# Performance work log

Hardware: AMD Instinct MI355X
Metric: run time of the kernel (lower is better)

## Reference

```python
import jax, jax.numpy as jnp
import numpy as np
from jax import lax

N_QUBITS = 4
DIM = 2 ** N_QUBITS  # 16-amplitude state vector


def _cnot_perm(c, t):
    # CNOT(control=c, target=t): amp_out[j] = amp_in[j ^ (bit_c(j) * mask_t)]
    idx = np.arange(DIM)
    mc = 1 << (N_QUBITS - 1 - c)  # PennyLane: wire 0 is most significant
    mt = 1 << (N_QUBITS - 1 - t)
    return jnp.asarray(np.where(idx & mc, idx ^ mt, idx))

# BasicEntanglerLayers ring pattern for n>2: CNOT(0,1),(1,2),(2,3),(3,0)
CNOT_PERMS = [_cnot_perm(i, (i + 1) % N_QUBITS) for i in range(N_QUBITS)]
_bits = (np.arange(DIM)[None, :] >> (N_QUBITS - 1 - np.arange(N_QUBITS)[:, None])) & 1
Z_SIGNS = jnp.asarray(1.0 - 2.0 * _bits, dtype=jnp.float32)  # [4,16], PauliZ eigenvalues


def _apply_1q(state, U, wire):
    # state: [B, 16] complex; U: [2,2] (shared) or [B,2,2] (per-sample angle)
    B = state.shape[0]
    s = state.reshape(B, 2 ** wire, 2, 2 ** (N_QUBITS - 1 - wire))
    if U.ndim == 2:
        s = jnp.einsum('ij,bajc->baic', U, s)
    else:
        s = jnp.einsum('bij,bajc->baic', U, s)
    return s.reshape(B, DIM)


def quantum_circuit(inputs, weights):
    # Batched default.qubit simulation. inputs: [B,4] angles, weights: [3,4].
    B = inputs.shape[0]
    state = jnp.zeros((B, DIM), jnp.complex64).at[:, 0].set(1.0)
    # RY(inputs[:,w]) on each wire (per-sample angles)
    for w in range(N_QUBITS):
        th = inputs[:, w] * 0.5
        c = jnp.cos(th).astype(jnp.complex64)
        s = jnp.sin(th).astype(jnp.complex64)
        U = jnp.stack([jnp.stack([c, -s], -1), jnp.stack([s, c], -1)], -2)  # [B,2,2]
        state = _apply_1q(state, U, w)
    # BasicEntanglerLayers: per layer, RX(weights[l,w]) on each wire then CNOT ring
    for l in range(weights.shape[0]):
        for w in range(N_QUBITS):
            th = weights[l, w] * 0.5
            cc = jnp.cos(th).astype(jnp.complex64)
            ss = (-1j) * jnp.sin(th).astype(jnp.complex64)
            U = jnp.stack([jnp.stack([cc, ss]), jnp.stack([ss, cc])])  # [2,2]
            state = _apply_1q(state, U, w)
        for w in range(N_QUBITS):
            state = state[:, CNOT_PERMS[w]]
    probs = jnp.abs(state) ** 2  # [B,16]
    return (probs @ Z_SIGNS.T).astype(jnp.float32)  # [B,4] <Z_w>


def setup_inputs() -> dict:
    key = jax.random.key(0)
    ks = jax.random.split(key, 8)
    B = 16384
    return {
        'x': jax.random.normal(ks[0], (B, 3, 32, 32), jnp.float32),
        'conv_w': jax.random.normal(ks[1], (N_QUBITS, 3, 3, 3), jnp.float32) * 0.1,
        'conv_b': jnp.zeros((N_QUBITS,), jnp.float32),
        'q_weights': jax.random.normal(ks[2], (3, N_QUBITS), jnp.float32),
        'w1': jax.random.normal(ks[3], (128, N_QUBITS), jnp.float32) * 0.1,
        'b1': jnp.zeros((128,), jnp.float32),
        'w2': jax.random.normal(ks[4], (3 * 32 * 32, 128), jnp.float32) * 0.05,
        'b2': jnp.zeros((3 * 32 * 32,), jnp.float32),
    }


def reference(x, conv_w, conv_b, q_weights, w1, b1, w2, b2):
    # Conv2d(3, 4, k=3, pad=1)
    y = lax.conv_general_dilated(
        x, conv_w, window_strides=(1, 1), padding='SAME',
        dimension_numbers=('NCHW', 'OIHW', 'NCHW')) + conv_b[None, :, None, None]
    # adaptive_avg_pool2d to (1,1) == global mean over H,W -> [B,4]
    pooled = y.mean(axis=(2, 3))
    # per-sample quantum circuit, batched; torch.tensor() in the original
    # detaches gradients, mirrored by stop_gradient
    q = lax.stop_gradient(quantum_circuit(pooled, q_weights))
    h = jax.nn.relu(q @ w1.T + b1)
    out = h @ w2.T + b2
    return out.reshape(-1, 3, 32, 32)
```

## Files before the change

### kernel.cpp

```cpp
#include <hip/hip_runtime.h>
#include <hip/hip_bf16.h>

typedef __attribute__((ext_vector_type(8))) short bf16x8;
typedef __attribute__((ext_vector_type(4))) float f32x4;

__device__ __forceinline__ unsigned short f2bf(float f) {
  union { __hip_bfloat16 b; unsigned short u; } cv;
  cv.b = __float2bfloat16(f);
  return cv.u;
}

__global__ __launch_bounds__(256) void k_cvt_w2(const float* __restrict__ w2,
                                                unsigned short* __restrict__ w2b) {
  const int i = (blockIdx.x * 256 + threadIdx.x) * 4;
  float4 v = *(const float4*)(w2 + i);
  union { uint2 u; unsigned short s[4]; } p;
  p.s[0] = f2bf(v.x); p.s[1] = f2bf(v.y); p.s[2] = f2bf(v.z); p.s[3] = f2bf(v.w);
  *(uint2*)(w2b + i) = p.u;
}

__global__ __launch_bounds__(64) void k_convpool(const float* __restrict__ x,
                                                 const float* __restrict__ cw,
                                                 const float* __restrict__ cb,
                                                 float* __restrict__ pooled) {
  const int b = blockIdx.x;
  const int t = threadIdx.x;
  const float4* x4 = (const float4*)x + (size_t)b * 768;
  float F[3] = {0,0,0}, R0[3] = {0,0,0}, R31[3] = {0,0,0}, C0[3] = {0,0,0}, C31[3] = {0,0,0};
  float k00[3] = {0,0,0}, k031[3] = {0,0,0}, k310[3] = {0,0,0}, k3131[3] = {0,0,0};
#pragma unroll
  for (int g = 0; g < 12; ++g) {
    const int i = g >> 2;
    const int p = (g & 3) * 64 + t;
    const int h = p >> 3;
    const int wq = p & 7;
    float4 f = x4[g * 64 + t];
    float sm = f.x + f.y + f.z + f.w;
    F[i] += sm;
    if (h == 0)  R0[i]  += sm;
    if (h == 31) R31[i] += sm;
    if (wq == 0) C0[i]  += f.x;
    if (wq == 7) C31[i] += f.w;
    if (p == 0)   k00[i]   = f.x;
    if (p == 7)   k031[i]  = f.w;
    if (p == 248) k310[i]  = f.x;
    if (p == 255) k3131[i] = f.w;
  }
#pragma unroll
  for (int i = 0; i < 3; ++i) {
#pragma unroll
    for (int off = 32; off; off >>= 1) {
      F[i]   += __shfl_xor(F[i], off);
      R0[i]  += __shfl_xor(R0[i], off);
      R31[i] += __shfl_xor(R31[i], off);
      C0[i]  += __shfl_xor(C0[i], off);
      C31[i] += __shfl_xor(C31[i], off);
    }
    k00[i]   = __shfl(k00[i], 0);
    k031[i]  = __shfl(k031[i], 7);
    k310[i]  = __shfl(k310[i], 56);
    k3131[i] = __shfl(k3131[i], 63);
  }
  if (t < 4) {
    const int o = t;
    float acc = 0.f;
#pragma unroll
    for (int i = 0; i < 3; ++i) {
      const float* wp = cw + (o * 3 + i) * 9;
      float w00 = wp[0], w01 = wp[1], w02 = wp[2];
      float w10 = wp[3], w11 = wp[4], w12 = wp[5];
      float w20 = wp[6], w21 = wp[7], w22 = wp[8];
      acc += (w00 + w01 + w02 + w10 + w11 + w12 + w20 + w21 + w22) * F[i];
      acc -= (w20 + w21 + w22) * R0[i];
      acc -= (w00 + w01 + w02) * R31[i];
      acc -= (w02 + w12 + w22) * C0[i];
      acc -= (w00 + w10 + w20) * C31[i];
      acc += w00 * k3131[i] + w02 * k310[i] + w20 * k031[i] + w22 * k00[i];
    }
    pooled[b * 4 + o] = cb[o] + acc * (1.0f / 1024.0f);
  }
}

__global__ __launch_bounds__(256) void k_qnn(const float* __restrict__ pooled,
                                             const float* __restrict__ qw,
                                             const float* __restrict__ w1,
                                             const float* __restrict__ b1,
                                             unsigned short* __restrict__ hout) {
  const int b = blockIdx.x * 256 + threadIdx.x;
  float4 pv = *((const float4*)pooled + b);
  float c[4], s[4];
  {
    float th[4] = {pv.x * 0.5f, pv.y * 0.5f, pv.z * 0.5f, pv.w * 0.5f};
#pragma unroll
    for (int w = 0; w < 4; ++w) { s[w] = sinf(th[w]); c[w] = cosf(th[w]); }
  }
  float sr[16], si[16];
#pragma unroll
  for (int k = 0; k < 16; ++k) {
    sr[k] = (k & 8 ? s[0] : c[0]) * (k & 4 ? s[1] : c[1]) *
            (k & 2 ? s[2] : c[2]) * (k & 1 ? s[3] : c[3]);
    si[k] = 0.f;
  }
#pragma unroll
  for (int l = 0; l < 3; ++l) {
#pragma unroll
    for (int w = 0; w < 4; ++w) {
      float th = qw[l * 4 + w] * 0.5f;
      float cc = cosf(th), ss = sinf(th);
      const int m = 1 << (3 - w);
#pragma unroll
      for (int k = 0; k < 16; ++k) {
        if (!(k & m)) {
          const int kb = k | m;
          float ar = sr[k], ai = si[k], br = sr[kb], bi = si[kb];
          sr[k]  = cc * ar + ss * bi;
          si[k]  = cc * ai - ss * br;
          sr[kb] = cc * br + ss * ai;
          si[kb] = cc * bi - ss * ar;
        }
      }
    }
#pragma unroll
    for (int w = 0; w < 4; ++w) {
      const int mc = 1 << (3 - w);
      const int mt = 1 << (3 - ((w + 1) & 3));
#pragma unroll
      for (int k = 0; k < 16; ++k) {
        if ((k & mc) && !(k & mt)) {
          const int kb = k | mt;
          float tr = sr[k]; sr[k] = sr[kb]; sr[kb] = tr;
          float ti = si[k]; si[k] = si[kb]; si[kb] = ti;
        }
      }
    }
  }
  float q[4] = {0.f, 0.f, 0.f, 0.f};
#pragma unroll
  for (int k = 0; k < 16; ++k) {
    float pr = sr[k] * sr[k] + si[k] * si[k];
#pragma unroll
    for (int w = 0; w < 4; ++w) q[w] += (k & (1 << (3 - w))) ? -pr : pr;
  }
#pragma unroll 1
  for (int jb = 0; jb < 16; ++jb) {
    union { uint4 u; unsigned short us[8]; } pack;
#pragma unroll
    for (int jj = 0; jj < 8; ++jj) {
      const int j = jb * 8 + jj;
      float4 wv = *((const float4*)w1 + j);
      float hv = b1[j] + wv.x * q[0] + wv.y * q[1] + wv.z * q[2] + wv.w * q[3];
      pack.us[jj] = f2bf(fmaxf(hv, 0.f));
    }
    ((uint4*)hout)[b * 16 + jb] = pack.u;
  }
}

__global__ __launch_bounds__(256) void k_gemm(const unsigned short* __restrict__ hA,
                                              const unsigned short* __restrict__ w2b,
                                              const float* __restrict__ b2,
                                              float* __restrict__ out) {
  const int bn = blockIdx.x * 64;
  const int bm = blockIdx.y * 64;
  const int t = threadIdx.x;
  const int lane = t & 63, wv = t >> 6;
  __shared__ unsigned short As[64][136];
  __shared__ unsigned short Bs[64][136];
  for (int cch = t; cch < 1024; cch += 256) {
    const int r = cch >> 4;
    const int col8 = (cch & 15) * 8;
    uint4 va = *(const uint4*)(hA + (size_t)(bm + r) * 128 + col8);
    *(uint4*)(&As[r][col8]) = va;
    uint4 vb = *(const uint4*)(w2b + (size_t)(bn + r) * 128 + col8);
    *(uint4*)(&Bs[r][col8]) = vb;
  }
  __syncthreads();
  f32x4 acc[4] = {{0,0,0,0},{0,0,0,0},{0,0,0,0},{0,0,0,0}};
  const int ar = wv * 16 + (lane & 15);
  const int kq = (lane >> 4) * 8;
#pragma unroll
  for (int ks = 0; ks < 4; ++ks) {
    bf16x8 a = *(const bf16x8*)(&As[ar][ks * 32 + kq]);
#pragma unroll
    for (int n = 0; n < 4; ++n) {
      bf16x8 bf = *(const bf16x8*)(&Bs[n * 16 + (lane & 15)][ks * 32 + kq]);
      acc[n] = __builtin_amdgcn_mfma_f32_16x16x32_bf16(a, bf, acc[n], 0, 0, 0);
    }
  }
  const int m0 = bm + wv * 16 + ((lane >> 4) << 2);
  const int c0 = bn + (lane & 15);
#pragma unroll
  for (int n = 0; n < 4; ++n) {
    const int col = c0 + n * 16;
    const float bias = b2[col];
#pragma unroll
    for (int j = 0; j < 4; ++j) {
      out[(size_t)(m0 + j) * 3072 + col] = acc[n][j] + bias;
    }
  }
}

extern "C" void kernel_launch(void* const* d_in, const int* in_sizes, int n_in,
                              void* d_out, int out_size, void* d_ws, size_t ws_size,
                              hipStream_t stream) {
  const float* x      = (const float*)d_in[0];
  const float* conv_w = (const float*)d_in[1];
  const float* conv_b = (const float*)d_in[2];
  const float* qw     = (const float*)d_in[3];
  const float* w1     = (const float*)d_in[4];
  const float* b1     = (const float*)d_in[5];
  const float* w2     = (const float*)d_in[6];
  const float* b2     = (const float*)d_in[7];
  float* out = (float*)d_out;

  const int B = in_sizes[0] / 3072;

  char* ws = (char*)d_ws;
  float* pooled        = (float*)ws;
  unsigned short* hbf  = (unsigned short*)(ws + (size_t)B * 16);
  unsigned short* w2b  = (unsigned short*)(ws + (size_t)B * 16 + (size_t)B * 256);

  hipLaunchKernelGGL(k_cvt_w2, dim3(384), dim3(256), 0, stream, w2, w2b);
  hipLaunchKernelGGL(k_convpool, dim3(B), dim3(64), 0, stream, x, conv_w, conv_b, pooled);
  hipLaunchKernelGGL(k_qnn, dim3(B / 256), dim3(256), 0, stream, pooled, qw, w1, b1, hbf);
  hipLaunchKernelGGL(k_gemm, dim3(48, B / 64), dim3(256), 0, stream, hbf, w2b, b2, out);
}
```

Measured before the change: 381.3 us.

## Swap MFMA operands for float4 output stores; retune convpool and qnn block sizes

```diff
diff --git a/kernel.cpp b/kernel.cpp
--- a/kernel.cpp
+++ b/kernel.cpp
@@ -19,12 +19,13 @@
   *(uint2*)(w2b + i) = p.u;
 }
 
-__global__ __launch_bounds__(64) void k_convpool(const float* __restrict__ x,
-                                                 const float* __restrict__ cw,
-                                                 const float* __restrict__ cb,
-                                                 float* __restrict__ pooled) {
-  const int b = blockIdx.x;
-  const int t = threadIdx.x;
+__global__ __launch_bounds__(256) void k_convpool(const float* __restrict__ x,
+                                                  const float* __restrict__ cw,
+                                                  const float* __restrict__ cb,
+                                                  float* __restrict__ pooled) {
+  const int wv = threadIdx.x >> 6;
+  const int b = blockIdx.x * 4 + wv;
+  const int t = threadIdx.x & 63;
   const float4* x4 = (const float4*)x + (size_t)b * 768;
   float F[3] = {0,0,0}, R0[3] = {0,0,0}, R31[3] = {0,0,0}, C0[3] = {0,0,0}, C31[3] = {0,0,0};
   float k00[3] = {0,0,0}, k031[3] = {0,0,0}, k310[3] = {0,0,0}, k3131[3] = {0,0,0};
@@ -81,12 +82,12 @@
   }
 }
 
-__global__ __launch_bounds__(256) void k_qnn(const float* __restrict__ pooled,
-                                             const float* __restrict__ qw,
-                                             const float* __restrict__ w1,
-                                             const float* __restrict__ b1,
-                                             unsigned short* __restrict__ hout) {
-  const int b = blockIdx.x * 256 + threadIdx.x;
+__global__ __launch_bounds__(64) void k_qnn(const float* __restrict__ pooled,
+                                            const float* __restrict__ qw,
+                                            const float* __restrict__ w1,
+                                            const float* __restrict__ b1,
+                                            unsigned short* __restrict__ hout) {
+  const int b = blockIdx.x * 64 + threadIdx.x;
   float4 pv = *((const float4*)pooled + b);
   float c[4], s[4];
   {
@@ -175,27 +176,29 @@
   }
   __syncthreads();
   f32x4 acc[4] = {{0,0,0,0},{0,0,0,0},{0,0,0,0},{0,0,0,0}};
-  const int ar = wv * 16 + (lane & 15);
+  const int mr = wv * 16 + (lane & 15);
   const int kq = (lane >> 4) * 8;
 #pragma unroll
   for (int ks = 0; ks < 4; ++ks) {
-    bf16x8 a = *(const bf16x8*)(&As[ar][ks * 32 + kq]);
+    bf16x8 hfrag = *(const bf16x8*)(&As[mr][ks * 32 + kq]);
 #pragma unroll
     for (int n = 0; n < 4; ++n) {
-      bf16x8 bf = *(const bf16x8*)(&Bs[n * 16 + (lane & 15)][ks * 32 + kq]);
-      acc[n] = __builtin_amdgcn_mfma_f32_16x16x32_bf16(a, bf, acc[n], 0, 0, 0);
-    }
-  }
-  const int m0 = bm + wv * 16 + ((lane >> 4) << 2);
-  const int c0 = bn + (lane & 15);
+      bf16x8 wfrag = *(const bf16x8*)(&Bs[n * 16 + (lane & 15)][ks * 32 + kq]);
+      acc[n] = __builtin_amdgcn_mfma_f32_16x16x32_bf16(wfrag, hfrag, acc[n], 0, 0, 0);
+    }
+  }
+  const int m = bm + wv * 16 + (lane & 15);
+  const int nq = (lane >> 4) << 2;
 #pragma unroll
   for (int n = 0; n < 4; ++n) {
-    const int col = c0 + n * 16;
-    const float bias = b2[col];
-#pragma unroll
-    for (int j = 0; j < 4; ++j) {
-      out[(size_t)(m0 + j) * 3072 + col] = acc[n][j] + bias;
-    }
+    const int n0 = bn + n * 16 + nq;
+    float4 bias = *(const float4*)(b2 + n0);
+    float4 o;
+    o.x = acc[n][0] + bias.x;
+    o.y = acc[n][1] + bias.y;
+    o.z = acc[n][2] + bias.z;
+    o.w = acc[n][3] + bias.w;
+    *(float4*)(out + (size_t)m * 3072 + n0) = o;
   }
 }
 
@@ -220,7 +223,7 @@
   unsigned short* w2b  = (unsigned short*)(ws + (size_t)B * 16 + (size_t)B * 256);
 
   hipLaunchKernelGGL(k_cvt_w2, dim3(384), dim3(256), 0, stream, w2, w2b);
-  hipLaunchKernelGGL(k_convpool, dim3(B), dim3(64), 0, stream, x, conv_w, conv_b, pooled);
-  hipLaunchKernelGGL(k_qnn, dim3(B / 256), dim3(256), 0, stream, pooled, qw, w1, b1, hbf);
+  hipLaunchKernelGGL(k_convpool, dim3(B / 4), dim3(256), 0, stream, x, conv_w, conv_b, pooled);
+  hipLaunchKernelGGL(k_qnn, dim3(B / 64), dim3(64), 0, stream, pooled, qw, w1, b1, hbf);
   hipLaunchKernelGGL(k_gemm, dim3(48, B / 64), dim3(256), 0, stream, hbf, w2b, b2, out);
 }
```

After: 393.0 us. 1.03x slower.
